# Optimization experiments

Measured on AMD Instinct MI355X. Metric: run time of the kernel, lower is better.

Reference implementation:

```python
import jax, jax.numpy as jnp
import numpy as np

N_BINS = 11
Q_LEN = 50
EMB = 50      # == dim_term_gating
BATCH = 256
D_LEN = 2000
EPS = 1e-8


def setup_inputs() -> dict:
    key = jax.random.key(0)
    ks = jax.random.split(key, 6)
    q_embeddings = jax.random.normal(ks[0], (BATCH, Q_LEN, EMB), jnp.float32)
    d_embeddings = jax.random.normal(ks[1], (BATCH, D_LEN, EMB), jnp.float32)
    q_embeddings_ids = jax.random.randint(ks[2], (BATCH, Q_LEN), 0, 30000)
    d_embeddings_ids = jax.random.randint(ks[3], (BATCH, D_LEN), 0, 30000)
    # linear1: Linear(n_bins*q_len, 1); gating: Linear(emb*q_len, 1, bias=False)
    W1 = jax.random.normal(ks[4], (N_BINS * Q_LEN,), jnp.float32) * 0.02
    b1 = jnp.zeros((1,), jnp.float32)
    Wg = jax.random.normal(ks[5], (EMB * Q_LEN,), jnp.float32) * 0.02
    return {
        "q_embeddings": q_embeddings,
        "d_embeddings": d_embeddings,
        "W1": W1,
        "b1": b1,
        "Wg": Wg,
        "q_embeddings_ids": q_embeddings_ids,
        "d_embeddings_ids": d_embeddings_ids,
    }


def reference(q_embeddings, d_embeddings, W1, b1, Wg, q_embeddings_ids, d_embeddings_ids):
    B, Q, E = q_embeddings.shape
    D = d_embeddings.shape[1]

    # ---- DrmmSimmat: cosine similarity between every query/doc term ----
    qn = q_embeddings / (jnp.linalg.norm(q_embeddings, axis=-1, keepdims=True) + EPS)
    dn = d_embeddings / (jnp.linalg.norm(d_embeddings, axis=-1, keepdims=True) + EPS)
    sim = jnp.einsum("bqe,bde->bqd", qn, dn)  # [B, Q, D]

    # ---- DrmmHistogram: per-query-term log-count histogram over [-1,1] ----
    # valid positions: token id != 0 (padding) in both query and doc dims
    valid = ((q_embeddings_ids > 0)[:, :, None] & (d_embeddings_ids > 0)[:, None, :])
    valid = valid.astype(jnp.float32)  # [B, Q, D]
    bins = jnp.clip(((sim + 1.000001) * 0.5 * (N_BINS - 1)).astype(jnp.int32), 0, N_BINS - 1)
    row = jnp.arange(B * Q, dtype=jnp.int32).reshape(B, Q, 1)  # histogram row per (b, q)
    flat_idx = (row * N_BINS + bins).reshape(-1)
    hist = jnp.zeros((B * Q * N_BINS,), jnp.float32).at[flat_idx].add(valid.reshape(-1))
    hist = jnp.log(hist + 1e-5).reshape(B, Q * N_BINS)

    # ---- feed-forward + term gating ----
    out_ffn = hist @ W1 + b1[0]                      # [B]
    gate = q_embeddings.reshape(B, Q * E) @ Wg       # [B]
    out_tgn = jax.nn.softmax(gate)                   # softmax over batch (faithful to F.softmax on squeezed [B])
    # torch broadcast (B,1)*(B,) -> (B,B); sum over dim=1
    matching_score = jnp.sum(out_ffn[:, None] * out_tgn[None, :], axis=1)  # [B]
    return matching_score
```

## Files before the change

### kernel.cpp

```cpp
#include <hip/hip_runtime.h>
#include <math.h>

#define BATCH 256
#define QL 50
#define EMB 50
#define DL 2000
#define NB 11
#define SEG 16
#define RPB 125
#define TPB 256
#define RSTRIDE 52
#define HB (QL * NB)

#define FOR_M5(M) M(0) M(1) M(2) M(3) M(4)
#define FOR_MN(M) \
  M(0,0) M(0,1) M(0,2) M(0,3) M(0,4) \
  M(1,0) M(1,1) M(1,2) M(1,3) M(1,4) \
  M(2,0) M(2,1) M(2,2) M(2,3) M(2,4) \
  M(3,0) M(3,1) M(3,2) M(3,3) M(3,4) \
  M(4,0) M(4,1) M(4,2) M(4,3) M(4,4)

#define DECL_ACC(m,n) float a_##m##_##n = 0.f;
#define LOAD_Q4(m) const float4 qv##m = *(const float4*)(qb0 + (m) * RSTRIDE + 4 * k);
#define LOAD_D4(n) const float4 dv##n = *(const float4*)(db0 + (n) * RSTRIDE + 4 * k);
#define LOAD_Q2(m) const float2 qt##m = *(const float2*)(qb0 + (m) * RSTRIDE + 48);
#define LOAD_D2(n) const float2 dt##n = *(const float2*)(db0 + (n) * RSTRIDE + 48);
#define FMA4(m,n) \
  a_##m##_##n = fmaf(qv##m.x, dv##n.x, a_##m##_##n); \
  a_##m##_##n = fmaf(qv##m.y, dv##n.y, a_##m##_##n); \
  a_##m##_##n = fmaf(qv##m.z, dv##n.z, a_##m##_##n); \
  a_##m##_##n = fmaf(qv##m.w, dv##n.w, a_##m##_##n);
#define FMA2T(m,n) \
  a_##m##_##n = fmaf(qt##m.x, dt##n.x, a_##m##_##n); \
  a_##m##_##n = fmaf(qt##m.y, dt##n.y, a_##m##_##n);
#define HIST_MN(m,n) if (qv_##m && dv_##n) { \
    const float s_  = a_##m##_##n * qrn##m * drn##n; \
    const float tt_ = ((s_ + 1.000001f) * 0.5f) * 10.0f; \
    int bb_ = (int)tt_; bb_ = bb_ < 0 ? 0 : (bb_ > 10 ? 10 : bb_); \
    atomicAdd(&s_hist[(qg5 + m) * NB + bb_], 1u); }

__global__ __launch_bounds__(TPB, 4)
void sim_hist_kernel(const float* __restrict__ de,
                     const int*   __restrict__ did,
                     const float* __restrict__ qe,
                     const int*   __restrict__ qid,
                     const float* __restrict__ Wg,
                     unsigned char* __restrict__ g_hist,
                     float* __restrict__ gate,
                     int* __restrict__ cnt)
{
    const int bid = blockIdx.x;
    const int b   = bid >> 4;
    const int seg = bid & 15;
    const int t   = threadIdx.x;

    __shared__ __align__(16) float s_d[RPB * RSTRIDE];
    __shared__ __align__(16) float s_q[QL * RSTRIDE];
    __shared__ float         s_drn[RPB];
    __shared__ float         s_qrn[QL];
    __shared__ unsigned char s_dval[RPB];
    __shared__ unsigned char s_qv[QL];
    __shared__ unsigned      s_hist[HB];
    __shared__ float         r2s[4];

    if (bid == 0 && t == 0) *cnt = 0;
    for (int i = t; i < HB; i += TPB) s_hist[i] = 0u;

    if (t < RPB) {
        const float* src = de + ((size_t)b * DL + seg * RPB + t) * EMB;
        float* dst = s_d + t * RSTRIDE;
        float ss = 0.f;
        #pragma unroll
        for (int ep = 0; ep < 25; ++ep) {
            const float2 v = *(const float2*)(src + 2 * ep);
            ss = fmaf(v.x, v.x, ss);
            ss = fmaf(v.y, v.y, ss);
            *(float2*)(dst + 2 * ep) = v;
        }
        s_drn[t]  = 1.0f / (sqrtf(ss) + 1e-8f);
        s_dval[t] = (did[(size_t)b * DL + seg * RPB + t] > 0) ? 1 : 0;
    } else if (t >= 128 && t < 128 + QL) {
        const int j = t - 128;
        const float* src = qe + ((size_t)b * QL + j) * EMB;
        float* dst = s_q + j * RSTRIDE;
        float ss = 0.f;
        #pragma unroll
        for (int ep = 0; ep < 25; ++ep) {
            const float2 v = *(const float2*)(src + 2 * ep);
            ss = fmaf(v.x, v.x, ss);
            ss = fmaf(v.y, v.y, ss);
            *(float2*)(dst + 2 * ep) = v;
        }
        s_qrn[j] = 1.0f / (sqrtf(ss) + 1e-8f);
        s_qv[j]  = (qid[(size_t)b * QL + j] > 0) ? 1 : 0;
    }
    __syncthreads();

    if (t < 250) {
        const int qg5 = (t % 10) * 5;
        const int rg5 = (t / 10) * 5;
        const float* qb0 = s_q + qg5 * RSTRIDE;
        const float* db0 = s_d + rg5 * RSTRIDE;
        FOR_MN(DECL_ACC)
        #pragma unroll 1
        for (int k = 0; k < 12; ++k) {
            FOR_M5(LOAD_Q4)
            FOR_M5(LOAD_D4)
            FOR_MN(FMA4)
        }
        {
            FOR_M5(LOAD_Q2)
            FOR_M5(LOAD_D2)
            FOR_MN(FMA2T)
        }
        const float qrn0 = s_qrn[qg5+0], qrn1 = s_qrn[qg5+1], qrn2 = s_qrn[qg5+2],
                    qrn3 = s_qrn[qg5+3], qrn4 = s_qrn[qg5+4];
        const float drn0 = s_drn[rg5+0], drn1 = s_drn[rg5+1], drn2 = s_drn[rg5+2],
                    drn3 = s_drn[rg5+3], drn4 = s_drn[rg5+4];
        const int qv_0 = s_qv[qg5+0], qv_1 = s_qv[qg5+1], qv_2 = s_qv[qg5+2],
                  qv_3 = s_qv[qg5+3], qv_4 = s_qv[qg5+4];
        const int dv_0 = s_dval[rg5+0], dv_1 = s_dval[rg5+1], dv_2 = s_dval[rg5+2],
                  dv_3 = s_dval[rg5+3], dv_4 = s_dval[rg5+4];
        FOR_MN(HIST_MN)
    }
    __syncthreads();

    unsigned char* hout = g_hist + ((size_t)b * SEG + seg) * HB;
    for (int i = t; i < HB; i += TPB) hout[i] = (unsigned char)s_hist[i];

    if (seg == 0) {
        const float* qbase = qe + (size_t)b * QL * EMB;
        float a2 = 0.f;
        for (int i = t; i < QL * EMB; i += TPB)
            a2 = fmaf(qbase[i], Wg[i], a2);
        #pragma unroll
        for (int off = 32; off > 0; off >>= 1) a2 += __shfl_down(a2, off, 64);
        if ((t & 63) == 0) r2s[t >> 6] = a2;
        __syncthreads();
        if (t == 0) gate[b] = r2s[0] + r2s[1] + r2s[2] + r2s[3];
    }
}

__global__ __launch_bounds__(TPB)
void ffn_score_kernel(const unsigned char* __restrict__ g_hist,
                      const float* __restrict__ W1,
                      const float* __restrict__ bias,
                      const float* __restrict__ gate,
                      float* __restrict__ ffn,
                      int* __restrict__ cnt,
                      float* __restrict__ out)
{
    const int b = blockIdx.x;
    const int t = threadIdx.x;
    const unsigned char* hb = g_hist + (size_t)b * SEG * HB;

    float a1 = 0.f;
    for (int i = t; i < HB; i += TPB) {
        unsigned c = 0;
        #pragma unroll
        for (int s = 0; s < SEG; ++s) c += hb[s * HB + i];
        a1 = fmaf(logf((float)c + 1e-5f), W1[i], a1);
    }
    #pragma unroll
    for (int off = 32; off > 0; off >>= 1) a1 += __shfl_down(a1, off, 64);
    __shared__ float r1s[4];
    __shared__ int   s_last;
    if ((t & 63) == 0) r1s[t >> 6] = a1;
    __syncthreads();
    if (t == 0) {
        const float v = r1s[0] + r1s[1] + r1s[2] + r1s[3] + bias[0];
        atomicExch(&ffn[b], v);
        __threadfence();
        const int old = atomicAdd(cnt, 1);
        s_last = (old == BATCH - 1) ? 1 : 0;
    }
    __syncthreads();
    if (!s_last) return;
    __threadfence();

    __shared__ float buf[4];
    __shared__ float sM, sZ, sS;
    const float g = gate[t];
    const float f = atomicAdd(&ffn[t], 0.0f);

    float m = g;
    #pragma unroll
    for (int off = 32; off > 0; off >>= 1) m = fmaxf(m, __shfl_down(m, off, 64));
    if ((t & 63) == 0) buf[t >> 6] = m;
    __syncthreads();
    if (t == 0) sM = fmaxf(fmaxf(buf[0], buf[1]), fmaxf(buf[2], buf[3]));
    __syncthreads();

    const float e = expf(g - sM);
    float z = e;
    #pragma unroll
    for (int off = 32; off > 0; off >>= 1) z += __shfl_down(z, off, 64);
    __syncthreads();
    if ((t & 63) == 0) buf[t >> 6] = z;
    __syncthreads();
    if (t == 0) sZ = buf[0] + buf[1] + buf[2] + buf[3];
    __syncthreads();

    const float p = e / sZ;
    float s = p;
    #pragma unroll
    for (int off = 32; off > 0; off >>= 1) s += __shfl_down(s, off, 64);
    __syncthreads();
    if ((t & 63) == 0) buf[t >> 6] = s;
    __syncthreads();
    if (t == 0) sS = buf[0] + buf[1] + buf[2] + buf[3];
    __syncthreads();

    out[t] = f * sS;
}

extern "C" void kernel_launch(void* const* d_in, const int* in_sizes, int n_in,
                              void* d_out, int out_size, void* d_ws, size_t ws_size,
                              hipStream_t stream)
{
    const float* qe  = (const float*)d_in[0];
    const float* de  = (const float*)d_in[1];
    const float* W1  = (const float*)d_in[2];
    const float* b1  = (const float*)d_in[3];
    const float* Wg  = (const float*)d_in[4];
    const int*   qid = (const int*)d_in[5];
    const int*   did = (const int*)d_in[6];
    float* out = (float*)d_out;

    char* ws = (char*)d_ws;
    unsigned char* g_hist = (unsigned char*)ws;
    float* gate = (float*)(ws + 2252800);
    float* ffn  = gate + BATCH;
    int*   cnt  = (int*)(ffn + BATCH);

    sim_hist_kernel<<<BATCH * SEG, TPB, 0, stream>>>(de, did, qe, qid, Wg,
                                                     g_hist, gate, cnt);
    ffn_score_kernel<<<BATCH, TPB, 0, stream>>>(g_hist, W1, b1, gate, ffn, cnt, out);
}
```

Measured before the change: 194.0 us.

## Split docs into 20 segments, pack histogram bytes, and coalesce the staging loads

```diff
diff --git a/kernel.cpp b/kernel.cpp
--- a/kernel.cpp
+++ b/kernel.cpp
@@ -6,25 +6,29 @@
 #define EMB 50
 #define DL 2000
 #define NB 11
-#define SEG 16
-#define RPB 125
+#define SEG 20
+#define RPB 100
 #define TPB 256
 #define RSTRIDE 52
 #define HB (QL * NB)
+#define HW 138
+#define HSTR 552
 
 #define FOR_M5(M) M(0) M(1) M(2) M(3) M(4)
+#define FOR_N4(M) M(0) M(1) M(2) M(3)
 #define FOR_MN(M) \
-  M(0,0) M(0,1) M(0,2) M(0,3) M(0,4) \
-  M(1,0) M(1,1) M(1,2) M(1,3) M(1,4) \
-  M(2,0) M(2,1) M(2,2) M(2,3) M(2,4) \
-  M(3,0) M(3,1) M(3,2) M(3,3) M(3,4) \
-  M(4,0) M(4,1) M(4,2) M(4,3) M(4,4)
+  M(0,0) M(0,1) M(0,2) M(0,3) \
+  M(1,0) M(1,1) M(1,2) M(1,3) \
+  M(2,0) M(2,1) M(2,2) M(2,3) \
+  M(3,0) M(3,1) M(3,2) M(3,3) \
+  M(4,0) M(4,1) M(4,2) M(4,3)
 
 #define DECL_ACC(m,n) float a_##m##_##n = 0.f;
-#define LOAD_Q4(m) const float4 qv##m = *(const float4*)(qb0 + (m) * RSTRIDE + 4 * k);
-#define LOAD_D4(n) const float4 dv##n = *(const float4*)(db0 + (n) * RSTRIDE + 4 * k);
-#define LOAD_Q2(m) const float2 qt##m = *(const float2*)(qb0 + (m) * RSTRIDE + 48);
-#define LOAD_D2(n) const float2 dt##n = *(const float2*)(db0 + (n) * RSTRIDE + 48);
+#define DB(n)  const float* db##n = s_d + (g + (n) * 25) * RSTRIDE;
+#define LQ(m)  const float4 qv##m = *(const float4*)(qb0 + (m) * RSTRIDE + o);
+#define LD(n)  const float4 dv##n = *(const float4*)(db##n + o);
+#define LQ2(m) const float2 qt##m = *(const float2*)(qb0 + (m) * RSTRIDE + 48);
+#define LD2(n) const float2 dt##n = *(const float2*)(db##n + 48);
 #define FMA4(m,n) \
   a_##m##_##n = fmaf(qv##m.x, dv##n.x, a_##m##_##n); \
   a_##m##_##n = fmaf(qv##m.y, dv##n.y, a_##m##_##n); \
@@ -33,13 +37,14 @@
 #define FMA2T(m,n) \
   a_##m##_##n = fmaf(qt##m.x, dt##n.x, a_##m##_##n); \
   a_##m##_##n = fmaf(qt##m.y, dt##n.y, a_##m##_##n);
-#define HIST_MN(m,n) if (qv_##m && dv_##n) { \
-    const float s_  = a_##m##_##n * qrn##m * drn##n; \
+#define HIST_MN(m,n) if (qs##m > 0.f && ds##n > 0.f) { \
+    const float s_  = a_##m##_##n * qs##m * ds##n; \
     const float tt_ = ((s_ + 1.000001f) * 0.5f) * 10.0f; \
     int bb_ = (int)tt_; bb_ = bb_ < 0 ? 0 : (bb_ > 10 ? 10 : bb_); \
-    atomicAdd(&s_hist[(qg5 + m) * NB + bb_], 1u); }
-
-__global__ __launch_bounds__(TPB, 4)
+    const int hidx_ = (qg5 + (m)) * NB + bb_; \
+    atomicAdd(&s_hist[hidx_ >> 2], 1u << ((hidx_ & 3) * 8)); }
+
+__global__ __launch_bounds__(TPB, 5)
 void sim_hist_kernel(const float* __restrict__ de,
                      const int*   __restrict__ did,
                      const float* __restrict__ qe,
@@ -50,83 +55,86 @@
                      int* __restrict__ cnt)
 {
     const int bid = blockIdx.x;
-    const int b   = bid >> 4;
-    const int seg = bid & 15;
+    const int b   = bid / SEG;
+    const int seg = bid - b * SEG;
     const int t   = threadIdx.x;
 
     __shared__ __align__(16) float s_d[RPB * RSTRIDE];
     __shared__ __align__(16) float s_q[QL * RSTRIDE];
-    __shared__ float         s_drn[RPB];
-    __shared__ float         s_qrn[QL];
-    __shared__ unsigned char s_dval[RPB];
-    __shared__ unsigned char s_qv[QL];
-    __shared__ unsigned      s_hist[HB];
-    __shared__ float         r2s[4];
+    __shared__ float    s_drn[RPB];
+    __shared__ float    s_qrn[QL];
+    __shared__ unsigned s_hist[HW];
+    __shared__ float    r2s[4];
 
     if (bid == 0 && t == 0) *cnt = 0;
-    for (int i = t; i < HB; i += TPB) s_hist[i] = 0u;
+    for (int i = t; i < HW; i += TPB) s_hist[i] = 0u;
+
+    const float2* dsrc = (const float2*)(de + ((size_t)b * DL + seg * RPB) * EMB);
+    for (int i = t; i < RPB * 25; i += TPB) {
+        const int r = i / 25, ep = i - r * 25;
+        ((float2*)(s_d + r * RSTRIDE))[ep] = dsrc[i];
+    }
+    const float2* qsrc = (const float2*)(qe + (size_t)b * QL * EMB);
+    for (int i = t; i < QL * 25; i += TPB) {
+        const int r = i / 25, ep = i - r * 25;
+        ((float2*)(s_q + r * RSTRIDE))[ep] = qsrc[i];
+    }
+    __syncthreads();
 
     if (t < RPB) {
-        const float* src = de + ((size_t)b * DL + seg * RPB + t) * EMB;
-        float* dst = s_d + t * RSTRIDE;
+        const float2* row = (const float2*)(s_d + t * RSTRIDE);
         float ss = 0.f;
         #pragma unroll
         for (int ep = 0; ep < 25; ++ep) {
-            const float2 v = *(const float2*)(src + 2 * ep);
+            const float2 v = row[ep];
             ss = fmaf(v.x, v.x, ss);
             ss = fmaf(v.y, v.y, ss);
-            *(float2*)(dst + 2 * ep) = v;
-        }
-        s_drn[t]  = 1.0f / (sqrtf(ss) + 1e-8f);
-        s_dval[t] = (did[(size_t)b * DL + seg * RPB + t] > 0) ? 1 : 0;
+        }
+        const float rn = 1.0f / (sqrtf(ss) + 1e-8f);
+        s_drn[t] = (did[(size_t)b * DL + seg * RPB + t] > 0) ? rn : -rn;
     } else if (t >= 128 && t < 128 + QL) {
         const int j = t - 128;
-        const float* src = qe + ((size_t)b * QL + j) * EMB;
-        float* dst = s_q + j * RSTRIDE;
+        const float2* row = (const float2*)(s_q + j * RSTRIDE);
         float ss = 0.f;
         #pragma unroll
         for (int ep = 0; ep < 25; ++ep) {
-            const float2 v = *(const float2*)(src + 2 * ep);
+            const float2 v = row[ep];
             ss = fmaf(v.x, v.x, ss);
             ss = fmaf(v.y, v.y, ss);
-            *(float2*)(dst + 2 * ep) = v;
-        }
-        s_qrn[j] = 1.0f / (sqrtf(ss) + 1e-8f);
-        s_qv[j]  = (qid[(size_t)b * QL + j] > 0) ? 1 : 0;
+        }
+        const float rn = 1.0f / (sqrtf(ss) + 1e-8f);
+        s_qrn[j] = (qid[(size_t)b * QL + j] > 0) ? rn : -rn;
     }
     __syncthreads();
 
     if (t < 250) {
         const int qg5 = (t % 10) * 5;
-        const int rg5 = (t / 10) * 5;
+        const int g   = t / 10;
         const float* qb0 = s_q + qg5 * RSTRIDE;
-        const float* db0 = s_d + rg5 * RSTRIDE;
+        FOR_N4(DB)
         FOR_MN(DECL_ACC)
         #pragma unroll 1
         for (int k = 0; k < 12; ++k) {
-            FOR_M5(LOAD_Q4)
-            FOR_M5(LOAD_D4)
+            const int o = 4 * k;
+            FOR_M5(LQ)
+            FOR_N4(LD)
             FOR_MN(FMA4)
         }
         {
-            FOR_M5(LOAD_Q2)
-            FOR_M5(LOAD_D2)
+            FOR_M5(LQ2)
+            FOR_N4(LD2)
             FOR_MN(FMA2T)
         }
-        const float qrn0 = s_qrn[qg5+0], qrn1 = s_qrn[qg5+1], qrn2 = s_qrn[qg5+2],
-                    qrn3 = s_qrn[qg5+3], qrn4 = s_qrn[qg5+4];
-        const float drn0 = s_drn[rg5+0], drn1 = s_drn[rg5+1], drn2 = s_drn[rg5+2],
-                    drn3 = s_drn[rg5+3], drn4 = s_drn[rg5+4];
-        const int qv_0 = s_qv[qg5+0], qv_1 = s_qv[qg5+1], qv_2 = s_qv[qg5+2],
-                  qv_3 = s_qv[qg5+3], qv_4 = s_qv[qg5+4];
-        const int dv_0 = s_dval[rg5+0], dv_1 = s_dval[rg5+1], dv_2 = s_dval[rg5+2],
-                  dv_3 = s_dval[rg5+3], dv_4 = s_dval[rg5+4];
+        const float qs0 = s_qrn[qg5+0], qs1 = s_qrn[qg5+1], qs2 = s_qrn[qg5+2],
+                    qs3 = s_qrn[qg5+3], qs4 = s_qrn[qg5+4];
+        const float ds0 = s_drn[g], ds1 = s_drn[g+25],
+                    ds2 = s_drn[g+50], ds3 = s_drn[g+75];
         FOR_MN(HIST_MN)
     }
     __syncthreads();
 
-    unsigned char* hout = g_hist + ((size_t)b * SEG + seg) * HB;
-    for (int i = t; i < HB; i += TPB) hout[i] = (unsigned char)s_hist[i];
+    unsigned* hout = (unsigned*)(g_hist + ((size_t)b * SEG + seg) * HSTR);
+    for (int i = t; i < HW; i += TPB) hout[i] = s_hist[i];
 
     if (seg == 0) {
         const float* qbase = qe + (size_t)b * QL * EMB;
@@ -152,13 +160,13 @@
 {
     const int b = blockIdx.x;
     const int t = threadIdx.x;
-    const unsigned char* hb = g_hist + (size_t)b * SEG * HB;
+    const unsigned char* hb = g_hist + (size_t)b * SEG * HSTR;
 
     float a1 = 0.f;
     for (int i = t; i < HB; i += TPB) {
         unsigned c = 0;
         #pragma unroll
-        for (int s = 0; s < SEG; ++s) c += hb[s * HB + i];
+        for (int s = 0; s < SEG; ++s) c += hb[s * HSTR + i];
         a1 = fmaf(logf((float)c + 1e-5f), W1[i], a1);
     }
     #pragma unroll
@@ -229,7 +237,7 @@
 
     char* ws = (char*)d_ws;
     unsigned char* g_hist = (unsigned char*)ws;
-    float* gate = (float*)(ws + 2252800);
+    float* gate = (float*)(ws + 2826240);
     float* ffn  = gate + BATCH;
     int*   cnt  = (int*)(ffn + BATCH);
 
```

After: 219.2 us. 13.0% more time.
